# Kernel tuning notes

Measured on AMD Instinct MI355X. Metric: run time of the kernel, lower is better.

The kernel has to match this reference:

```python
import jax, jax.numpy as jnp
import numpy as np

N_NODES = 100000
N_EDGES = 1600000
N_GRAPHS = 512
IN_DIM = 128
HID = 128
N_CLASSES = 10


def _gcn_conv(x, W, b, src, dst, n):
    """PyG GCNConv: out = D^{-1/2} (A+I) D^{-1/2} (x @ W) + b."""
    xw = x @ W  # [n, out_dim]
    loop = jnp.arange(n)
    s = jnp.concatenate([src, loop])  # add self loops
    d = jnp.concatenate([dst, loop])
    deg = jax.ops.segment_sum(jnp.ones(s.shape, dtype=xw.dtype), d, num_segments=n)
    dinv = jnp.where(deg > 0, jax.lax.rsqrt(deg), jnp.zeros((), xw.dtype))
    norm = dinv[s] * dinv[d]  # [E + n]
    out = jax.ops.segment_sum(xw[s] * norm[:, None], d, num_segments=n)
    return out + b


def _global_mean_pool(x, batch, num_graphs):
    sums = jax.ops.segment_sum(x, batch, num_segments=num_graphs)
    cnts = jax.ops.segment_sum(jnp.ones(batch.shape, dtype=x.dtype), batch, num_segments=num_graphs)
    return sums / jnp.maximum(cnts, 1.0)[:, None]


def setup_inputs() -> dict:
    key = jax.random.key(0)
    ks = jax.random.split(key, 8)
    x = jax.random.normal(ks[0], (N_NODES, IN_DIM), dtype=jnp.float32)
    edge_index = jax.random.randint(ks[1], (2, N_EDGES), 0, N_NODES, dtype=jnp.int64)
    batch = jnp.sort(jax.random.randint(ks[2], (N_NODES,), 0, N_GRAPHS, dtype=jnp.int64))
    sc = 1.0 / np.sqrt(IN_DIM)
    W1 = jax.random.normal(ks[3], (IN_DIM, HID), dtype=jnp.float32) * sc
    b1 = jnp.zeros((HID,), dtype=jnp.float32)
    W2 = jax.random.normal(ks[4], (HID, HID), dtype=jnp.float32) * (1.0 / np.sqrt(HID))
    b2 = jnp.zeros((HID,), dtype=jnp.float32)
    Wc = jax.random.normal(ks[5], (HID, N_CLASSES), dtype=jnp.float32) * (1.0 / np.sqrt(HID))
    bc = jnp.zeros((N_CLASSES,), dtype=jnp.float32)
    return {"x": x, "edge_index": edge_index, "batch": batch,
            "W1": W1, "b1": b1, "W2": W2, "b2": b2, "Wc": Wc, "bc": bc}


def reference(x, edge_index, batch, W1, b1, W2, b2, Wc, bc):
    src, dst = edge_index[0], edge_index[1]
    n = x.shape[0]
    h = _gcn_conv(x, W1, b1, src, dst, n)
    h = jax.nn.relu(h)
    h = _gcn_conv(h, W2, b2, src, dst, n)
    g = _global_mean_pool(h, batch, N_GRAPHS)
    return g @ Wc + bc
```

## Files before the change

kernel.cpp:

```cpp
#include <hip/hip_runtime.h>

#define N_NODES 100000
#define N_EDGES 1600000
#define N_GRAPHS 512
#define DIM 128
#define NCLS 10
#define NBKT 782
#define BCAP 2560

typedef __attribute__((ext_vector_type(8))) short short8;
typedef __attribute__((ext_vector_type(4))) float f32x4;

static __device__ __forceinline__ unsigned short f2bf(float f) {
    unsigned u = __float_as_uint(f);
    unsigned r = (u + 0x7FFF + ((u >> 16) & 1)) >> 16;
    return (unsigned short)r;
}
static __device__ __forceinline__ float bf2f(unsigned u) {
    return __uint_as_float(u << 16);
}


__global__ void k_wprep(const float* __restrict__ W1, const float* __restrict__ W2,
                        unsigned short* __restrict__ wf1, unsigned short* __restrict__ wf2,
                        int* __restrict__ bcnt) {
    int b = blockIdx.x;
    if (b >= 128) {
        int i = (b - 128) * 256 + threadIdx.x;
        if (i < NBKT) bcnt[i] = 0;
        return;
    }
    const float* W = (b < 64) ? W1 : W2;
    unsigned short* wfrag = (b < 64) ? wf1 : wf2;
    int t = (b & 63) * 256 + threadIdx.x;
    int j = t & 7, lane = (t >> 3) & 63, nt = (t >> 9) & 7, kit = t >> 12;
    int k = kit * 32 + (lane >> 4) * 8 + j;
    int n = nt * 16 + (lane & 15);
    float v = W[k * 128 + n];
    unsigned short h = f2bf(v);
    wfrag[t] = h;
    wfrag[16384 + t] = f2bf(v - bf2f(h));
}


__global__ __launch_bounds__(256) void k_bucket(
    const int* __restrict__ src, const int* __restrict__ dst,
    int* __restrict__ bcnt, unsigned* __restrict__ bpack, int E) {
    __shared__ int cnt[NBKT];
    __shared__ int base[NBKT];
    int tid = threadIdx.x;
    for (int i = tid; i < NBKT; i += 256) cnt[i] = 0;
    __syncthreads();
    int e0 = blockIdx.x * 4096 + tid;
    unsigned pk[16]; short bk[16];
#pragma unroll
    for (int j = 0; j < 16; j++) {
        int e = e0 + j * 256;
        if (e < E) {
            int s = src[e], d = dst[e];
            bk[j] = (short)(d >> 7);
            pk[j] = ((unsigned)(d & 127) << 17) | (unsigned)s;
            atomicAdd(&cnt[bk[j]], 1);
        } else bk[j] = -1;
    }
    __syncthreads();
    for (int i = tid; i < NBKT; i += 256) {
        int c = cnt[i];
        base[i] = c ? atomicAdd(&bcnt[i], c) : 0;
        cnt[i] = 0;
    }
    __syncthreads();
#pragma unroll
    for (int j = 0; j < 16; j++) {
        if (bk[j] >= 0) {
            int p = base[bk[j]] + atomicAdd(&cnt[bk[j]], 1);
            if (p < BCAP) bpack[(size_t)bk[j] * BCAP + p] = pk[j];
        }
    }
}


static __device__ __forceinline__ void bsort_body(
    char* smemraw, int b,
    const unsigned* __restrict__ bpack, const int* __restrict__ bcnt,
    int* __restrict__ rp, float* __restrict__ dinv,
    int* __restrict__ esrc, int N, float* __restrict__ dvs) {
    int* lds      = (int*)smemraw;
    int* cnt      = lds + 256;
    int* scan     = lds + 384;
    int* cur      = lds + 512;
    int* gbase_sh = lds + 640;
    int tid = threadIdx.x;
    int v[4], pre[4];
    int s = 0;
#pragma unroll
    for (int j = 0; j < 4; j++) {
        int idx = tid * 4 + j;
        v[j] = (idx < NBKT) ? min(bcnt[idx], BCAP) : 0;
        pre[j] = s; s += v[j];
    }
    lds[tid] = s;
    __syncthreads();
    for (int off = 1; off < 256; off <<= 1) {
        int t = (tid >= off) ? lds[tid - off] : 0;
        __syncthreads();
        lds[tid] += t;
        __syncthreads();
    }
    if (tid == (b >> 2)) *gbase_sh = lds[tid] - s + pre[b & 3];
    if (tid < 128) cnt[tid] = 0;
    __syncthreads();
    int gbase = *gbase_sh;
    int n0 = b << 7;
    int m = min(bcnt[b], BCAP);
    const unsigned* bp = bpack + (size_t)b * BCAP;
    for (int j = tid; j < m; j += 256) atomicAdd(&cnt[bp[j] >> 17], 1);
    __syncthreads();
    if (tid < 128) scan[tid] = cnt[tid];
    __syncthreads();
    for (int off = 1; off < 128; off <<= 1) {
        int t = (tid < 128 && tid >= off) ? scan[tid - off] : 0;
        __syncthreads();
        if (tid < 128) scan[tid] += t;
        __syncthreads();
    }
    if (tid < 128) {
        int c = cnt[tid];
        int excl = scan[tid] - c;
        int node = n0 + tid;
        float dv = rsqrtf((float)(c + 1));
        if (node <= N) rp[node] = gbase + excl;
        if (node < N) dinv[node] = dv;
        dvs[tid] = dv;
        cur[tid] = gbase + excl;
    }
    __syncthreads();
    for (int j = tid; j < m; j += 256) {
        unsigned pk = bp[j];
        int p = atomicAdd(&cur[pk >> 17], 1);
        esrc[p] = (int)(pk & 0x1FFFF);
    }
}

static __device__ __forceinline__ void gemm_f32_body(
    char* smemraw, int rowBlk,
    const float* __restrict__ A, const unsigned short* __restrict__ wfrag,
    const float* __restrict__ dvs, unsigned short* __restrict__ ybf, int M) {
    unsigned short* ldsw = (unsigned short*)smemraw;
    int tid = threadIdx.x, wave = tid >> 6, lane = tid & 63;
    int m = lane & 15, quad = lane >> 4;
    int rowBase = rowBlk * 128 + wave * 32;
    int r0 = rowBase + m, r1 = rowBase + 16 + m;
    for (int i = tid; i < 2048; i += 256)
        ((short8*)ldsw)[i] = ((const short8*)wfrag)[i];
    __syncthreads();
    f32x4 acc0[8], acc1[8];
#pragma unroll
    for (int i = 0; i < 8; i++) { acc0[i] = (f32x4){0,0,0,0}; acc1[i] = (f32x4){0,0,0,0}; }
    const unsigned short* wlo = wfrag + 16384;

#pragma unroll
    for (int kit = 0; kit < 4; kit++) {
        float a0[8], a1[8];
        if (r0 < M) {
            const float4* ap = (const float4*)(A + (size_t)r0 * 128 + kit * 32 + quad * 8);
            float4 f0 = ap[0], f1 = ap[1];
            a0[0]=f0.x; a0[1]=f0.y; a0[2]=f0.z; a0[3]=f0.w; a0[4]=f1.x; a0[5]=f1.y; a0[6]=f1.z; a0[7]=f1.w;
        } else { for (int j = 0; j < 8; j++) a0[j] = 0.f; }
        if (r1 < M) {
            const float4* ap = (const float4*)(A + (size_t)r1 * 128 + kit * 32 + quad * 8);
            float4 f0 = ap[0], f1 = ap[1];
            a1[0]=f0.x; a1[1]=f0.y; a1[2]=f0.z; a1[3]=f0.w; a1[4]=f1.x; a1[5]=f1.y; a1[6]=f1.z; a1[7]=f1.w;
        } else { for (int j = 0; j < 8; j++) a1[j] = 0.f; }
        short8 ahi0, alo0, ahi1, alo1;
#pragma unroll
        for (int j = 0; j < 8; j++) {
            unsigned short h0 = f2bf(a0[j]);
            ahi0[j] = (short)h0; alo0[j] = (short)f2bf(a0[j] - bf2f(h0));
            unsigned short h1 = f2bf(a1[j]);
            ahi1[j] = (short)h1; alo1[j] = (short)f2bf(a1[j] - bf2f(h1));
        }
        int fb = kit * 4096 + lane * 8;
#pragma unroll
        for (int nt = 0; nt < 8; nt++) {
            int idx = fb + nt * 512;
            short8 bhi = *(const short8*)(ldsw + idx);
            short8 blo = *(const short8*)(wlo + idx);
            acc0[nt] = __builtin_amdgcn_mfma_f32_16x16x32_bf16(ahi0, bhi, acc0[nt], 0, 0, 0);
            acc0[nt] = __builtin_amdgcn_mfma_f32_16x16x32_bf16(alo0, bhi, acc0[nt], 0, 0, 0);
            acc0[nt] = __builtin_amdgcn_mfma_f32_16x16x32_bf16(ahi0, blo, acc0[nt], 0, 0, 0);
            acc1[nt] = __builtin_amdgcn_mfma_f32_16x16x32_bf16(ahi1, bhi, acc1[nt], 0, 0, 0);
            acc1[nt] = __builtin_amdgcn_mfma_f32_16x16x32_bf16(alo1, bhi, acc1[nt], 0, 0, 0);
            acc1[nt] = __builtin_amdgcn_mfma_f32_16x16x32_bf16(ahi1, blo, acc1[nt], 0, 0, 0);
        }
    }
    __syncthreads();
    unsigned short* wsm = ldsw + wave * 32 * 136;
#pragma unroll
    for (int rg = 0; rg < 4; rg++) {
        float s0 = dvs[wave * 32 + quad * 4 + rg];
        float s1 = dvs[wave * 32 + 16 + quad * 4 + rg];
#pragma unroll
        for (int nt = 0; nt < 8; nt++) {
            wsm[(quad * 4 + rg) * 136 + nt * 16 + m] = f2bf(acc0[nt][rg] * s0);
            wsm[(16 + quad * 4 + rg) * 136 + nt * 16 + m] = f2bf(acc1[nt][rg] * s1);
        }
    }
    __syncthreads();
#pragma unroll
    for (int i = 0; i < 8; i++) {
        int rl = i * 4 + quad;
        int grow = rowBase + rl;
        if (grow < M) {
            short8 v = *(const short8*)(wsm + rl * 136 + m * 8);
            *(short8*)(ybf + (size_t)grow * 128 + m * 8) = v;
        }
    }
}


__global__ __launch_bounds__(256) void k_fuse(
    const unsigned* __restrict__ bpack, const int* __restrict__ bcnt,
    int* __restrict__ rp, float* __restrict__ dinv, int* __restrict__ esrc, int N,
    const float* __restrict__ A, const unsigned short* __restrict__ wfrag,
    unsigned short* __restrict__ ybf, int M) {
    __shared__ __align__(16) char smem[4 * 32 * 136 * 2];
    __shared__ float dvs[128];
    int b = blockIdx.x;
    bsort_body(smem, b, bpack, bcnt, rp, dinv, esrc, N, dvs);
    __syncthreads();
    gemm_f32_body(smem, b, A, wfrag, dvs, ybf, M);
}


__global__ __launch_bounds__(512) void k_aggemm(
    const unsigned short* __restrict__ y, const float* __restrict__ dinv,
    const int* __restrict__ rp, const int* __restrict__ esrc,
    const float* __restrict__ bias, const unsigned short* __restrict__ wfrag,
    unsigned short* __restrict__ ybf, int N) {
    __shared__ unsigned short h1[128 * 136];
    __shared__ unsigned short ldsw[16384];
    __shared__ float dvs[128];
    int tid = threadIdx.x, wave = tid >> 6, lane = tid & 63;
    int slab = blockIdx.x * 128;

    for (int i = tid; i < 2048; i += 512)
        ((short8*)ldsw)[i] = ((const short8*)wfrag)[i];

    const unsigned* y2 = (const unsigned*)y;
    float2 bv = ((const float2*)bias)[lane];
    for (int i = 0; i < 16; i++) {
        int local = wave * 16 + i;
        int node = slab + local;
        unsigned packed = 0;
        float sd = 0.f;
        if (node < N) {
            sd = dinv[node];
            unsigned vs = y2[(size_t)node * 64 + lane];
            float a0 = bf2f(vs & 0xFFFF), a1 = bf2f(vs >> 16);
            int beg = rp[node], end = rp[node + 1];
            int j = beg;
            while (j < end) {
                int idxv = (j + lane < end) ? esrc[j + lane] : 0;
                int cnt = end - j; if (cnt > 64) cnt = 64;
                int ii = 0;
                for (; ii + 4 <= cnt; ii += 4) {
                    int s0 = __shfl(idxv, ii + 0);
                    int s1 = __shfl(idxv, ii + 1);
                    int s2 = __shfl(idxv, ii + 2);
                    int s3 = __shfl(idxv, ii + 3);
                    unsigned v0 = y2[(size_t)s0 * 64 + lane];
                    unsigned v1 = y2[(size_t)s1 * 64 + lane];
                    unsigned v2 = y2[(size_t)s2 * 64 + lane];
                    unsigned v3 = y2[(size_t)s3 * 64 + lane];
                    a0 += bf2f(v0 & 0xFFFF); a1 += bf2f(v0 >> 16);
                    a0 += bf2f(v1 & 0xFFFF); a1 += bf2f(v1 >> 16);
                    a0 += bf2f(v2 & 0xFFFF); a1 += bf2f(v2 >> 16);
                    a0 += bf2f(v3 & 0xFFFF); a1 += bf2f(v3 >> 16);
                }
                for (; ii < cnt; ii++) {
                    int s = __shfl(idxv, ii);
                    unsigned v = y2[(size_t)s * 64 + lane];
                    a0 += bf2f(v & 0xFFFF); a1 += bf2f(v >> 16);
                }
                j += cnt;
            }
            float o0 = fmaxf(sd * a0 + bv.x, 0.f);
            float o1 = fmaxf(sd * a1 + bv.y, 0.f);
            packed = (unsigned)f2bf(o0) | ((unsigned)f2bf(o1) << 16);
        }
        *(unsigned*)&h1[local * 136 + lane * 2] = packed;
        if (lane == 0) dvs[local] = sd;
    }
    __syncthreads();

    int m = lane & 15, quad = lane >> 4;
    int rowLocal = wave * 16;
    f32x4 acc[8];
#pragma unroll
    for (int i = 0; i < 8; i++) acc[i] = (f32x4){0,0,0,0};
    const unsigned short* wlo = wfrag + 16384;
#pragma unroll
    for (int kit = 0; kit < 4; kit++) {
        short8 ah = *(const short8*)(h1 + (rowLocal + m) * 136 + kit * 32 + quad * 8);
        int fb = kit * 4096 + lane * 8;
#pragma unroll
        for (int nt = 0; nt < 8; nt++) {
            int idx = fb + nt * 512;
            short8 bhi = *(const short8*)(ldsw + idx);
            short8 blo = *(const short8*)(wlo + idx);
            acc[nt] = __builtin_amdgcn_mfma_f32_16x16x32_bf16(ah, bhi, acc[nt], 0, 0, 0);
            acc[nt] = __builtin_amdgcn_mfma_f32_16x16x32_bf16(ah, blo, acc[nt], 0, 0, 0);
        }
    }
    unsigned short* wsm = h1 + rowLocal * 136;
#pragma unroll
    for (int rg = 0; rg < 4; rg++) {
        float s0 = dvs[rowLocal + quad * 4 + rg];
#pragma unroll
        for (int nt = 0; nt < 8; nt++) {
            wsm[(quad * 4 + rg) * 136 + nt * 16 + m] = f2bf(acc[nt][rg] * s0);
        }
    }
#pragma unroll
    for (int i = 0; i < 4; i++) {
        int rl = i * 4 + quad;
        int grow = slab + rowLocal + rl;
        if (grow < N) {
            short8 v = *(const short8*)(wsm + rl * 136 + m * 8);
            *(short8*)(ybf + (size_t)grow * 128 + m * 8) = v;
        }
    }
}


__global__ __launch_bounds__(256) void k_agg(
    const unsigned short* __restrict__ y, const float* __restrict__ dinv,
    const int* __restrict__ rp, const int* __restrict__ esrc,
    const float* __restrict__ bias, unsigned* __restrict__ out, int relu, int N) {
    int wave = threadIdx.x >> 6;
    int lane = threadIdx.x & 63;
    int node = blockIdx.x * 4 + wave;
    if (node >= N) return;
    const unsigned* y2 = (const unsigned*)y;
    unsigned vs = y2[(size_t)node * 64 + lane];
    float a0 = bf2f(vs & 0xFFFF), a1 = bf2f(vs >> 16);
    int beg = rp[node], end = rp[node + 1];
    int j = beg;
    while (j < end) {
        int idxv = (j + lane < end) ? esrc[j + lane] : 0;
        int cnt = end - j; if (cnt > 64) cnt = 64;
        int i = 0;
        for (; i + 4 <= cnt; i += 4) {
            int s0 = __shfl(idxv, i + 0);
            int s1 = __shfl(idxv, i + 1);
            int s2 = __shfl(idxv, i + 2);
            int s3 = __shfl(idxv, i + 3);
            unsigned v0 = y2[(size_t)s0 * 64 + lane];
            unsigned v1 = y2[(size_t)s1 * 64 + lane];
            unsigned v2 = y2[(size_t)s2 * 64 + lane];
            unsigned v3 = y2[(size_t)s3 * 64 + lane];
            a0 += bf2f(v0 & 0xFFFF); a1 += bf2f(v0 >> 16);
            a0 += bf2f(v1 & 0xFFFF); a1 += bf2f(v1 >> 16);
            a0 += bf2f(v2 & 0xFFFF); a1 += bf2f(v2 >> 16);
            a0 += bf2f(v3 & 0xFFFF); a1 += bf2f(v3 >> 16);
        }
        for (; i < cnt; i++) {
            int s = __shfl(idxv, i);
            unsigned v = y2[(size_t)s * 64 + lane];
            a0 += bf2f(v & 0xFFFF); a1 += bf2f(v >> 16);
        }
        j += cnt;
    }
    float s = dinv[node];
    float2 bv = ((const float2*)bias)[lane];
    float o0 = s * a0 + bv.x;
    float o1 = s * a1 + bv.y;
    if (relu) { o0 = fmaxf(o0, 0.f); o1 = fmaxf(o1, 0.f); }
    out[(size_t)node * 64 + lane] = (unsigned)f2bf(o0) | ((unsigned)f2bf(o1) << 16);
}


__global__ __launch_bounds__(256) void k_poolhead(
    const unsigned* __restrict__ h2, const int* __restrict__ batch,
    const float* __restrict__ Wc, const float* __restrict__ bc,
    float* __restrict__ out, int n) {
    __shared__ float2 red[4][64];
    __shared__ float grow[DIM];
    int gid = blockIdx.x;
    int tid = threadIdx.x, wave = tid >> 6, lane = tid & 63;
    int lo = 0, hi = n;
    while (lo < hi) { int mid = (lo + hi) >> 1; if (batch[mid] < gid) lo = mid + 1; else hi = mid; }
    int start = lo;
    hi = n;
    while (lo < hi) { int mid = (lo + hi) >> 1; if (batch[mid] < gid + 1) lo = mid + 1; else hi = mid; }
    int end = lo;
    float a0 = 0.f, a1 = 0.f;
    for (int r = start + wave; r < end; r += 4) {
        unsigned v = h2[(size_t)r * 64 + lane];
        a0 += bf2f(v & 0xFFFF); a1 += bf2f(v >> 16);
    }
    red[wave][lane] = make_float2(a0, a1);
    __syncthreads();
    if (tid < 64) {
        float2 s = red[0][tid];
        s.x += red[1][tid].x; s.y += red[1][tid].y;
        s.x += red[2][tid].x; s.y += red[2][tid].y;
        s.x += red[3][tid].x; s.y += red[3][tid].y;
        int cnt = end - start;
        float inv = 1.f / (float)(cnt > 0 ? cnt : 1);
        grow[tid * 2] = s.x * inv;
        grow[tid * 2 + 1] = s.y * inv;
    }
    __syncthreads();
    if (tid < NCLS) {
        float acc = bc[tid];
#pragma unroll 16
        for (int k = 0; k < DIM; k++) acc += grow[k] * Wc[k * NCLS + tid];
        out[gid * NCLS + tid] = acc;
    }
}

extern "C" void kernel_launch(void* const* d_in, const int* in_sizes, int n_in,
                              void* d_out, int out_size, void* d_ws, size_t ws_size,
                              hipStream_t stream) {
    const float* x    = (const float*)d_in[0];
    const int*   ei   = (const int*)d_in[1];
    const int*   batch= (const int*)d_in[2];
    const float* W1   = (const float*)d_in[3];
    const float* b1   = (const float*)d_in[4];
    const float* W2   = (const float*)d_in[5];
    const float* b2   = (const float*)d_in[6];
    const float* Wc   = (const float*)d_in[7];
    const float* bc   = (const float*)d_in[8];
    float* out = (float*)d_out;
    const int N = N_NODES, E = N_EDGES;
    const int* src = ei;
    const int* dst = ei + E;

    char* ws = (char*)d_ws;
    size_t off = 0;
    auto carve = [&](size_t bytes) -> void* {
        void* p = ws + off;
        off = (off + bytes + 255) & ~(size_t)255;
        return p;
    };
    int*      rp    = (int*)     carve((size_t)(N + 1) * 4);
    float*    dinv  = (float*)   carve((size_t)N * 4);
    int*      bcnt  = (int*)     carve(NBKT * 4);
    unsigned* bpack = (unsigned*)carve((size_t)NBKT * BCAP * 4);
    int*      esrc  = (int*)     carve((size_t)E * 4);
    unsigned short* wf1 = (unsigned short*)carve(2 * 16384 * 2);
    unsigned short* wf2 = (unsigned short*)carve(2 * 16384 * 2);
    unsigned short* bufY = (unsigned short*)carve((size_t)N * DIM * 2);
    unsigned short* bufH = (unsigned short*)carve((size_t)N * DIM * 2);
    (void)ws_size; (void)n_in; (void)in_sizes; (void)out_size;

    const int nbBkt = (E + 4095) / 4096;

    hipLaunchKernelGGL(k_wprep,  dim3(128 + (NBKT + 255) / 256), dim3(256), 0, stream, W1, W2, wf1, wf2, bcnt);
    hipLaunchKernelGGL(k_bucket, dim3(nbBkt), dim3(256), 0, stream, src, dst, bcnt, bpack, E);
    hipLaunchKernelGGL(k_fuse, dim3(NBKT), dim3(256), 0, stream,
                       bpack, bcnt, rp, dinv, esrc, N, x, wf1, bufY, N);
    hipLaunchKernelGGL(k_aggemm, dim3(NBKT), dim3(512), 0, stream,
                       bufY, dinv, rp, esrc, b1, wf2, bufH, N);
    hipLaunchKernelGGL(k_agg, dim3((N + 3) / 4), dim3(256), 0, stream, bufH, dinv, rp, esrc, b2, (unsigned*)bufY, 0, N);
    hipLaunchKernelGGL(k_poolhead, dim3(N_GRAPHS), dim3(256), 0, stream, (const unsigned*)bufY, batch, Wc, bc, out, N);
}
```

Before: 359.6 us.

## Shrink fused aggregate+GEMM tiles to 32 rows with column-split MFMA across waves

The layer-2 fused aggregation+GEMM kernel moves from 128-node blocks of 512 threads to 32-node blocks of 256 threads, with about 3125 blocks instead of 782. LDS use drops from about 67KB to about 8.7KB, and the weight fragments are read straight from global/L2 instead of being staged in LDS. Each wave now computes two 16-column tiles for all 32 rows rather than all columns for 16 rows. The aim is higher occupancy and more waves in flight to hide the latency of the irregular gathers, at the cost of more repeated weight reads and extra barriers.

```diff
diff --git a/kernel.cpp b/kernel.cpp
--- a/kernel.cpp
+++ b/kernel.cpp
@@ -233,29 +233,22 @@
 }
 
 
-__global__ __launch_bounds__(512) void k_aggemm(
+__global__ __launch_bounds__(256) void k_aggemm2(
     const unsigned short* __restrict__ y, const float* __restrict__ dinv,
     const int* __restrict__ rp, const int* __restrict__ esrc,
     const float* __restrict__ bias, const unsigned short* __restrict__ wfrag,
     unsigned short* __restrict__ ybf, int N) {
-    __shared__ unsigned short h1[128 * 136];
-    __shared__ unsigned short ldsw[16384];
-    __shared__ float dvs[128];
+    __shared__ unsigned h1[32 * 68];
     int tid = threadIdx.x, wave = tid >> 6, lane = tid & 63;
-    int slab = blockIdx.x * 128;
-
-    for (int i = tid; i < 2048; i += 512)
-        ((short8*)ldsw)[i] = ((const short8*)wfrag)[i];
-
+    int slab = blockIdx.x * 32;
     const unsigned* y2 = (const unsigned*)y;
     float2 bv = ((const float2*)bias)[lane];
-    for (int i = 0; i < 16; i++) {
-        int local = wave * 16 + i;
-        int node = slab + local;
+
+    for (int ni = 0; ni < 8; ni++) {
+        int lr = wave * 8 + ni;
+        int node = slab + lr;
         unsigned packed = 0;
-        float sd = 0.f;
         if (node < N) {
-            sd = dinv[node];
             unsigned vs = y2[(size_t)node * 64 + lane];
             float a0 = bf2f(vs & 0xFFFF), a1 = bf2f(vs >> 16);
             int beg = rp[node], end = rp[node + 1];
@@ -263,12 +256,12 @@
             while (j < end) {
                 int idxv = (j + lane < end) ? esrc[j + lane] : 0;
                 int cnt = end - j; if (cnt > 64) cnt = 64;
-                int ii = 0;
-                for (; ii + 4 <= cnt; ii += 4) {
-                    int s0 = __shfl(idxv, ii + 0);
-                    int s1 = __shfl(idxv, ii + 1);
-                    int s2 = __shfl(idxv, ii + 2);
-                    int s3 = __shfl(idxv, ii + 3);
+                int i = 0;
+                for (; i + 4 <= cnt; i += 4) {
+                    int s0 = __shfl(idxv, i + 0);
+                    int s1 = __shfl(idxv, i + 1);
+                    int s2 = __shfl(idxv, i + 2);
+                    int s3 = __shfl(idxv, i + 3);
                     unsigned v0 = y2[(size_t)s0 * 64 + lane];
                     unsigned v1 = y2[(size_t)s1 * 64 + lane];
                     unsigned v2 = y2[(size_t)s2 * 64 + lane];
@@ -278,57 +271,67 @@
                     a0 += bf2f(v2 & 0xFFFF); a1 += bf2f(v2 >> 16);
                     a0 += bf2f(v3 & 0xFFFF); a1 += bf2f(v3 >> 16);
                 }
-                for (; ii < cnt; ii++) {
-                    int s = __shfl(idxv, ii);
+                for (; i < cnt; i++) {
+                    int s = __shfl(idxv, i);
                     unsigned v = y2[(size_t)s * 64 + lane];
                     a0 += bf2f(v & 0xFFFF); a1 += bf2f(v >> 16);
                 }
                 j += cnt;
             }
-            float o0 = fmaxf(sd * a0 + bv.x, 0.f);
-            float o1 = fmaxf(sd * a1 + bv.y, 0.f);
+            float s = dinv[node];
+            float o0 = fmaxf(s * a0 + bv.x, 0.f);
+            float o1 = fmaxf(s * a1 + bv.y, 0.f);
             packed = (unsigned)f2bf(o0) | ((unsigned)f2bf(o1) << 16);
         }
-        *(unsigned*)&h1[local * 136 + lane * 2] = packed;
-        if (lane == 0) dvs[local] = sd;
-    }
-    __syncthreads();
-
+        h1[lr * 68 + lane] = packed;
+    }
+    __syncthreads();
+
+    const unsigned short* h1us = (const unsigned short*)h1;
     int m = lane & 15, quad = lane >> 4;
-    int rowLocal = wave * 16;
-    f32x4 acc[8];
-#pragma unroll
-    for (int i = 0; i < 8; i++) acc[i] = (f32x4){0,0,0,0};
+    f32x4 acc0[2], acc1[2];
+#pragma unroll
+    for (int i = 0; i < 2; i++) { acc0[i] = (f32x4){0,0,0,0}; acc1[i] = (f32x4){0,0,0,0}; }
     const unsigned short* wlo = wfrag + 16384;
 #pragma unroll
     for (int kit = 0; kit < 4; kit++) {
-        short8 ah = *(const short8*)(h1 + (rowLocal + m) * 136 + kit * 32 + quad * 8);
-        int fb = kit * 4096 + lane * 8;
-#pragma unroll
-        for (int nt = 0; nt < 8; nt++) {
-            int idx = fb + nt * 512;
-            short8 bhi = *(const short8*)(ldsw + idx);
+        short8 ah0 = *(const short8*)(h1us + m * 136 + kit * 32 + quad * 8);
+        short8 ah1 = *(const short8*)(h1us + (16 + m) * 136 + kit * 32 + quad * 8);
+#pragma unroll
+        for (int ct = 0; ct < 2; ct++) {
+            int idx = kit * 4096 + lane * 8 + (wave * 2 + ct) * 512;
+            short8 bhi = *(const short8*)(wfrag + idx);
             short8 blo = *(const short8*)(wlo + idx);
-            acc[nt] = __builtin_amdgcn_mfma_f32_16x16x32_bf16(ah, bhi, acc[nt], 0, 0, 0);
-            acc[nt] = __builtin_amdgcn_mfma_f32_16x16x32_bf16(ah, blo, acc[nt], 0, 0, 0);
-        }
-    }
-    unsigned short* wsm = h1 + rowLocal * 136;
+            acc0[ct] = __builtin_amdgcn_mfma_f32_16x16x32_bf16(ah0, bhi, acc0[ct], 0, 0, 0);
+            acc0[ct] = __builtin_amdgcn_mfma_f32_16x16x32_bf16(ah0, blo, acc0[ct], 0, 0, 0);
+            acc1[ct] = __builtin_amdgcn_mfma_f32_16x16x32_bf16(ah1, bhi, acc1[ct], 0, 0, 0);
+            acc1[ct] = __builtin_amdgcn_mfma_f32_16x16x32_bf16(ah1, blo, acc1[ct], 0, 0, 0);
+        }
+    }
+    float dv0 = (slab + m < N) ? dinv[slab + m] : 0.f;
+    float dv1 = (slab + 16 + m < N) ? dinv[slab + 16 + m] : 0.f;
+    __syncthreads();
+    unsigned short* wsm = (unsigned short*)h1;
 #pragma unroll
     for (int rg = 0; rg < 4; rg++) {
-        float s0 = dvs[rowLocal + quad * 4 + rg];
-#pragma unroll
-        for (int nt = 0; nt < 8; nt++) {
-            wsm[(quad * 4 + rg) * 136 + nt * 16 + m] = f2bf(acc[nt][rg] * s0);
-        }
-    }
-#pragma unroll
-    for (int i = 0; i < 4; i++) {
-        int rl = i * 4 + quad;
-        int grow = slab + rowLocal + rl;
+        float s0 = __shfl(dv0, quad * 4 + rg);
+        float s1 = __shfl(dv1, quad * 4 + rg);
+#pragma unroll
+        for (int ct = 0; ct < 2; ct++) {
+            int colb = (wave * 2 + ct) * 16 + m;
+            wsm[(quad * 4 + rg) * 136 + colb] = f2bf(acc0[ct][rg] * s0);
+            wsm[(16 + quad * 4 + rg) * 136 + colb] = f2bf(acc1[ct][rg] * s1);
+        }
+    }
+    __syncthreads();
+#pragma unroll
+    for (int pass = 0; pass < 2; pass++) {
+        int flat = pass * 256 + tid;
+        int rl = flat >> 4, c8 = flat & 15;
+        int grow = slab + rl;
         if (grow < N) {
-            short8 v = *(const short8*)(wsm + rl * 136 + m * 8);
-            *(short8*)(ybf + (size_t)grow * 128 + m * 8) = v;
+            short8 v = *(const short8*)(wsm + rl * 136 + c8 * 8);
+            *(short8*)(ybf + (size_t)grow * 128 + c8 * 8) = v;
         }
     }
 }
@@ -462,7 +465,7 @@
     hipLaunchKernelGGL(k_bucket, dim3(nbBkt), dim3(256), 0, stream, src, dst, bcnt, bpack, E);
     hipLaunchKernelGGL(k_fuse, dim3(NBKT), dim3(256), 0, stream,
                        bpack, bcnt, rp, dinv, esrc, N, x, wf1, bufY, N);
-    hipLaunchKernelGGL(k_aggemm, dim3(NBKT), dim3(512), 0, stream,
+    hipLaunchKernelGGL(k_aggemm2, dim3((N + 31) / 32), dim3(256), 0, stream,
                        bufY, dinv, rp, esrc, b1, wf2, bufH, N);
     hipLaunchKernelGGL(k_agg, dim3((N + 3) / 4), dim3(256), 0, stream, bufH, dinv, rp, esrc, b2, (unsigned*)bufY, 0, N);
     hipLaunchKernelGGL(k_poolhead, dim3(N_GRAPHS), dim3(256), 0, stream, (const unsigned*)bufY, batch, Wc, bc, out, N);
```

After: 325.3 us. -9.6%, faster.
